# Performance work log

Measured on AMD Instinct MI355X. Metric: run time of the kernel, lower is better.

Reference implementation:

```python
import jax, jax.numpy as jnp
import numpy as np

B = 128      # puzzles per batch
CELLS = 81
N = B * CELLS
H = 96       # hidden_dim
E_SZ = 16    # embed_size
T = 16       # num_steps


def _sudoku_edges():
    r = np.arange(CELLS) // 9
    c = np.arange(CELLS) % 9
    b = (r // 3) * 3 + (c // 3)
    src, dst = [], []
    for u in range(CELLS):
        for v in range(CELLS):
            if u != v and (r[u] == r[v] or c[u] == c[v] or b[u] == b[v]):
                src.append(u)
                dst.append(v)
    return np.asarray(src, np.int32), np.asarray(dst, np.int32)


def setup_inputs() -> dict:
    key = jax.random.key(0)
    ks = jax.random.split(key, 24)
    s, d = _sudoku_edges()
    off = (np.arange(B, dtype=np.int32) * CELLS)[:, None]
    src = jnp.asarray((s[None, :] + off).reshape(-1))
    dst = jnp.asarray((d[None, :] + off).reshape(-1))
    row = jnp.asarray(np.tile(np.arange(CELLS, dtype=np.int32) // 9, B))
    col = jnp.asarray(np.tile(np.arange(CELLS, dtype=np.int32) % 9, B))
    q = jax.random.randint(ks[0], (N,), 0, 10, dtype=jnp.int32)
    labels = jax.random.randint(ks[1], (N,), 1, 10, dtype=jnp.int32)

    def lin(k, o, i):
        return (jax.random.normal(k, (o, i), jnp.float32) / np.sqrt(i)).astype(jnp.float32)

    d_emb = jax.random.normal(ks[2], (10, E_SZ), jnp.float32)
    r_emb = jax.random.normal(ks[3], (9, E_SZ), jnp.float32)
    c_emb = jax.random.normal(ks[4], (9, E_SZ), jnp.float32)
    in_W0 = lin(ks[5], H, 3 * E_SZ)
    in_W = jnp.stack([lin(ks[6 + i], H, H) for i in range(3)])   # [3,H,H]
    in_b = jnp.zeros((4, H), jnp.float32)
    msg_W0 = lin(ks[9], H, 2 * H)
    msg_W = jnp.stack([lin(ks[10 + i], H, H) for i in range(3)])
    msg_b = jnp.zeros((4, H), jnp.float32)
    # LSTMCell (no bias): input = cat(x, m) of size 2H, hidden H; gate order i,f,g,o
    W_ih = lin(ks[13], 4 * H, 2 * H)
    W_hh = lin(ks[14], 4 * H, H)
    out_W = lin(ks[15], 10, H)
    out_b = jnp.zeros((10,), jnp.float32)
    return dict(q=q, row=row, col=col, labels=labels, src=src, dst=dst,
                d_emb=d_emb, r_emb=r_emb, c_emb=c_emb,
                in_W0=in_W0, in_W=in_W, in_b=in_b,
                msg_W0=msg_W0, msg_W=msg_W, msg_b=msg_b,
                W_ih=W_ih, W_hh=W_hh, out_W=out_W, out_b=out_b)


def _mlp4(x, W0, W, b):
    # Linear,ReLU,Linear,ReLU,Linear,ReLU,Linear
    x = jax.nn.relu(x @ W0.T + b[0])
    x = jax.nn.relu(x @ W[0].T + b[1])
    x = jax.nn.relu(x @ W[1].T + b[2])
    return x @ W[2].T + b[3]


def reference(q, row, col, labels, src, dst, d_emb, r_emb, c_emb,
              in_W0, in_W, in_b, msg_W0, msg_W, msg_b,
              W_ih, W_hh, out_W, out_b):
    x = _mlp4(jnp.concatenate([d_emb[q], r_emb[row], c_emb[col]], -1),
              in_W0, in_W, in_b)                       # [N,H]
    h0 = x
    rh0 = jnp.zeros_like(x)
    rc0 = jnp.zeros_like(x)

    def step(carry, _):
        h, rh, rc = carry
        # per-edge message: MLP(cat(h_src, h_dst)), sum-aggregated into dst
        me = _mlp4(jnp.concatenate([h[src], h[dst]], -1), msg_W0, msg_W, msg_b)
        m = jax.ops.segment_sum(me, dst, num_segments=N)  # [N,H]
        gates = jnp.concatenate([x, m], -1) @ W_ih.T + rh @ W_hh.T
        i, f, g, o = jnp.split(gates, 4, axis=-1)
        nc = jax.nn.sigmoid(f) * rc + jax.nn.sigmoid(i) * jnp.tanh(g)
        nh = jax.nn.sigmoid(o) * jnp.tanh(nc)
        return (nh, nh, nc), nh

    _, hs = jax.lax.scan(step, (h0, rh0, rc0), None, length=T)  # [T,N,H]
    logits = hs @ out_W.T + out_b                               # [T,N,10]
    preds = jnp.argmax(logits, -1)                              # [T,N]
    lf = logits.reshape(-1, 10)
    lab = jnp.tile(labels, T)
    logp = jax.nn.log_softmax(lf, -1)
    loss = -jnp.mean(jnp.take_along_axis(logp, lab[:, None].astype(jnp.int32), 1))
    return preds, loss, lf
```

## Files before the change

kernel.cpp:

```cpp
#include <hip/hip_runtime.h>

#define NN 10368
#define EE 207360
#define TT 16

#define O_W0AT    0
#define O_W0BT    9216
#define O_WHHT    18432
#define O_WIHXT   55296
#define O_WCOMBT  92160
#define O_GB      129024
#define O_LOSS    129408
#define O_WIN0T   129424
#define O_WINT    134032
#define O_H       161680
#define O_C       (O_H  + NN*96)
#define O_A       (O_C  + NN*96)
#define O_BV      (O_A  + NN*96)
#define O_S2      (O_BV + NN*96)
#define O_X       (O_S2 + NN*96)
#define O_WFRAG   (O_X  + NN*96)
#define O_GX      (O_WFRAG + 27648)
#define O_WL2     O_X
#define O_WAB2    (O_X + 110592)

using bf16x8 = __attribute__((ext_vector_type(8))) short;
using f32x4  = __attribute__((ext_vector_type(4))) float;

__device__ __forceinline__ float sigm(float x){ return 1.f/(1.f + expf(-x)); }

__device__ __forceinline__ unsigned rne_bf16(float f){
  unsigned u = __float_as_uint(f);
  u += 0x7fffu + ((u >> 16) & 1u);
  return u >> 16;
}
__device__ __forceinline__ void split3(float x, short& h, short& m, short& l){
  unsigned uh = rne_bf16(x); h = (short)uh;
  float fh = __uint_as_float(uh << 16);
  float r1 = x - fh;
  unsigned um = rne_bf16(r1); m = (short)um;
  float fm = __uint_as_float(um << 16);
  float r2 = r1 - fm;
  l = (short)rne_bf16(r2);
}

__device__ __forceinline__ f32x4 mfma6(bf16x8 aH, bf16x8 aM, bf16x8 aL,
                                       bf16x8 WH, bf16x8 WM, bf16x8 WL, f32x4 acc){
  acc = __builtin_amdgcn_mfma_f32_16x16x32_bf16(aH, WH, acc, 0,0,0);
  acc = __builtin_amdgcn_mfma_f32_16x16x32_bf16(aH, WM, acc, 0,0,0);
  acc = __builtin_amdgcn_mfma_f32_16x16x32_bf16(aM, WH, acc, 0,0,0);
  acc = __builtin_amdgcn_mfma_f32_16x16x32_bf16(aH, WL, acc, 0,0,0);
  acc = __builtin_amdgcn_mfma_f32_16x16x32_bf16(aL, WH, acc, 0,0,0);
  acc = __builtin_amdgcn_mfma_f32_16x16x32_bf16(aM, WM, acc, 0,0,0);
  return acc;
}

__global__ void k_convert(float* ws, const float* msgW0, const float* Whh, const float* Wih,
                          const float* inW0, const float* inW)
{
  int i = blockIdx.x*256 + threadIdx.x;
  if (i < 9216){ int k=i/96, j=i%96; ws[O_W0AT+i] = msgW0[j*192+k];    return; } i -= 9216;
  if (i < 9216){ int k=i/96, j=i%96; ws[O_W0BT+i] = msgW0[j*192+96+k]; return; } i -= 9216;
  if (i < 36864){ int k=i/384, j=i%384; ws[O_WHHT+i]  = Whh[j*96+k];   return; } i -= 36864;
  if (i < 36864){ int k=i/384, j=i%384; ws[O_WIHXT+i] = Wih[j*192+k];  return; } i -= 36864;
  if (i < 4608){ int k=i/96, j=i%96; ws[O_WIN0T+i] = inW0[j*48+k];     return; } i -= 4608;
  if (i < 27648){ int l=i/9216, r=i%9216; int k=r/96, j=r%96;
                  ws[O_WINT+i] = inW[l*9216 + j*96 + k];               return; } i -= 27648;
  if (i == 0){ ws[O_LOSS] = 0.f; }
}

__global__ void k_wfrag(float* ws, const float* msgW)
{
  int idx = blockIdx.x*256 + threadIdx.x;
  if (idx >= 2*3*18*64) return;
  int lane = idx & 63;
  int tile = (idx >> 6) % 18;
  int lev  = (idx >> 6) / 18 % 3;
  int layer= (idx >> 6) / 54;
  int nt = tile/3, kt = tile%3;
  int nout = (lane & 15) + 16*nt;
  int q = lane >> 4;
  unsigned short* wf = (unsigned short*)(ws + O_WFRAG);
  unsigned short* dstp = wf + (size_t)(((layer*3+lev)*18 + tile)*64 + lane)*8;
  const float* W = msgW + layer*9216;
  for (int j=0;j<8;j++){
    float wv = W[nout*96 + 32*kt + 8*q + j];
    short h,m,l; split3(wv, h, m, l);
    dstp[j] = (unsigned short)(lev==0 ? h : (lev==1 ? m : l));
  }
}

__global__ void k_wcomb(float* ws, const float* Wih, const float* msgW, const float* msgb)
{
  int t = blockIdx.x*256 + threadIdx.x;
  if (t >= 36864) return;
  int j = t % 384, qq = t / 384;
  float a0=0.f,a1=0.f,a2=0.f,a3=0.f;
  for (int r=0;r<96;r+=4){
    a0 = fmaf(Wih[j*192+96+r  ], msgW[2*9216+(r  )*96+qq], a0);
    a1 = fmaf(Wih[j*192+96+r+1], msgW[2*9216+(r+1)*96+qq], a1);
    a2 = fmaf(Wih[j*192+96+r+2], msgW[2*9216+(r+2)*96+qq], a2);
    a3 = fmaf(Wih[j*192+96+r+3], msgW[2*9216+(r+3)*96+qq], a3);
  }
  ws[O_WCOMBT + qq*384 + j] = (a0+a1)+(a2+a3);
  if (qq == 0){
    float g=0.f;
    for (int r=0;r<96;r++) g = fmaf(Wih[j*192+96+r], msgb[288+r], g);
    ws[O_GB + j] = 20.f * g;
  }
}

__global__ void k_wl(float* ws)
{
  int idx = blockIdx.x*256 + threadIdx.x;
  if (idx >= 24*6*64) return;
  int L  = idx & 63;
  int ks = (idx >> 6) % 6;
  int nt = (idx >> 6) / 6;
  int col = (L & 15) + 16*nt;
  int q = L >> 4;
  unsigned short* wf = (unsigned short*)(ws + O_WL2);
  for (int j=0;j<8;j++){
    int k = 32*(ks%3) + 8*q + j;
    float wv = (ks < 3) ? ws[O_WCOMBT + k*384 + col] : ws[O_WHHT + k*384 + col];
    short h,m,l; split3(wv, h, m, l);
    wf[(size_t)(((0*24+nt)*6 + ks)*64 + L)*8 + j] = (unsigned short)h;
    wf[(size_t)(((1*24+nt)*6 + ks)*64 + L)*8 + j] = (unsigned short)m;
    wf[(size_t)(((2*24+nt)*6 + ks)*64 + L)*8 + j] = (unsigned short)l;
  }
}

__global__ void k_wab(float* ws)
{
  int idx = blockIdx.x*256 + threadIdx.x;
  if (idx >= 12*3*64) return;
  int L  = idx & 63;
  int ks = (idx >> 6) % 3;
  int nt = (idx >> 6) / 3;
  int col = (L & 15) + 16*nt;
  int q = L >> 4;
  unsigned short* wf = (unsigned short*)(ws + O_WAB2);
  for (int j=0;j<8;j++){
    int k = 32*ks + 8*q + j;
    float wv = (col < 96) ? ws[O_W0AT + k*96 + col] : ws[O_W0BT + k*96 + (col-96)];
    short h,m,l; split3(wv, h, m, l);
    wf[(size_t)(((0*12+nt)*3 + ks)*64 + L)*8 + j] = (unsigned short)h;
    wf[(size_t)(((1*12+nt)*3 + ks)*64 + L)*8 + j] = (unsigned short)m;
    wf[(size_t)(((2*12+nt)*3 + ks)*64 + L)*8 + j] = (unsigned short)l;
  }
}

__global__ __launch_bounds__(192) void k_input(float* ws,
    const int* q, const int* row, const int* col,
    const float* demb, const float* remb, const float* cemb,
    const float* inb, const float* msgb)
{
  __shared__ float ein[2][8*49];
  __shared__ float hb[2][8*97];
  int tid = threadIdx.x; int g = tid/96, j = tid%96;
  int nq = blockIdx.x*2 + g; int n0 = nq*8;

  for (int idx=j; idx<384; idx+=96){
    int i = idx/48, f = idx%48; int n = n0+i;
    float v;
    if (f < 16)      v = demb[q[n]*16 + f];
    else if (f < 32) v = remb[row[n]*16 + (f-16)];
    else             v = cemb[col[n]*16 + (f-32)];
    ein[g][i*49+f] = v;
  }
  __syncthreads();

  float acc[8];
  {
    const float* W0T = ws + O_WIN0T;
    float b0 = inb[j];
    #pragma unroll
    for (int i=0;i<8;i++) acc[i]=b0;
    #pragma unroll 2
    for (int k=0;k<48;k++){
      float w = W0T[k*96+j];
      #pragma unroll
      for (int i=0;i<8;i++) acc[i] = fmaf(w, ein[g][i*49+k], acc[i]);
    }
    #pragma unroll
    for (int i=0;i<8;i++) hb[g][i*97+j] = fmaxf(acc[i], 0.f);
  }
  __syncthreads();

  for (int l=0;l<3;l++){
    const float* WT = ws + O_WINT + l*9216;
    float bl = inb[(l+1)*96 + j];
    #pragma unroll
    for (int i=0;i<8;i++) acc[i]=bl;
    #pragma unroll 2
    for (int k=0;k<96;k++){
      float w = WT[k*96+j];
      #pragma unroll
      for (int i=0;i<8;i++) acc[i] = fmaf(w, hb[g][i*97+k], acc[i]);
    }
    __syncthreads();
    if (l < 2){
      #pragma unroll
      for (int i=0;i<8;i++) hb[g][i*97+j] = fmaxf(acc[i], 0.f);
    } else {
      #pragma unroll
      for (int i=0;i<8;i++) hb[g][i*97+j] = acc[i];
    }
    __syncthreads();
  }

  float* h = ws + O_H; float* c = ws + O_C; float* x = ws + O_X;
  #pragma unroll
  for (int i=0;i<8;i++){
    int n = n0+i;
    float vv = hb[g][i*97+j];
    h[n*96+j]=vv; x[n*96+j]=vv; c[n*96+j]=0.f;
  }
  const float* WA = ws + O_W0AT; const float* WB = ws + O_W0BT;
  float aa[8], ab[8];
  #pragma unroll
  for (int i=0;i<8;i++){ aa[i]=0.f; ab[i]=0.f; }
  #pragma unroll 2
  for (int k=0;k<96;k++){
    float wa=WA[k*96+j], wb=WB[k*96+j];
    #pragma unroll
    for (int i=0;i<8;i++){
      float hv = hb[g][i*97+k];
      aa[i]=fmaf(wa,hv,aa[i]); ab[i]=fmaf(wb,hv,ab[i]);
    }
  }
  float* A=ws+O_A; float* Bv=ws+O_BV;
  float b0v = msgb[j];
  #pragma unroll
  for (int i=0;i<8;i++){ int n=n0+i; A[n*96+j]=aa[i]; Bv[n*96+j]=ab[i]+b0v; }
}

__global__ __launch_bounds__(384) void k_gx(float* ws)
{
  __shared__ float sx[768];
  int tid = threadIdx.x;
  int nb = blockIdx.x*8;
  for (int idx = tid; idx < 768; idx += 384)
    sx[idx] = ws[O_X + (size_t)nb*96 + idx];
  float gb = ws[O_GB + tid];
  __syncthreads();
  const float* WX = ws + O_WIHXT;
  float acc[8];
  #pragma unroll
  for (int i=0;i<8;i++) acc[i] = gb;
  #pragma unroll 2
  for (int k0=0;k0<96;k0+=4){
    float4 xv[8];
    #pragma unroll
    for (int i=0;i<8;i++) xv[i] = *(const float4*)&sx[i*96+k0];
    #pragma unroll
    for (int kk=0;kk<4;kk++){
      float w = WX[(k0+kk)*384 + tid];
      #pragma unroll
      for (int i=0;i<8;i++){
        float xe = (kk==0)?xv[i].x:(kk==1)?xv[i].y:(kk==2)?xv[i].z:xv[i].w;
        acc[i] = fmaf(w, xe, acc[i]);
      }
    }
  }
  #pragma unroll
  for (int i=0;i<8;i++)
    ws[O_GX + (size_t)(nb+i)*384 + tid] = acc[i];
}

__global__ __launch_bounds__(384) void k_edge(float* ws, const int* dst, const float* msgb)
{
  __shared__ bf16x8 aF[45][64];
  int tid = threadIdx.x;
  int w = tid >> 6, L = tid & 63;
  int q = L >> 4, m = L & 15;
  int n0 = blockIdx.x*4;
  int e0 = blockIdx.x*80;
  const unsigned short* wf = (const unsigned short*)(ws + O_WFRAG);
  const float* Aact = ws + O_A;
  const float* Bact = ws + O_BV;

  for (int idx = tid; idx < 960; idx += 384){
    int mt = idx / 192;
    int kt = (idx % 192) / 64;
    int Ls = idx & 63;
    int el = mt*16 + (Ls & 15);
    int v  = dst[e0 + el];
    int n  = n0 + el/20;
    int k0 = 32*kt + 8*(Ls >> 4);
    float4 a0 = *(const float4*)(Aact + (size_t)v*96 + k0);
    float4 a1 = *(const float4*)(Aact + (size_t)v*96 + k0 + 4);
    float4 b0 = *(const float4*)(Bact + (size_t)n*96 + k0);
    float4 b1 = *(const float4*)(Bact + (size_t)n*96 + k0 + 4);
    float r[8];
    r[0]=fmaxf(a0.x+b0.x,0.f); r[1]=fmaxf(a0.y+b0.y,0.f);
    r[2]=fmaxf(a0.z+b0.z,0.f); r[3]=fmaxf(a0.w+b0.w,0.f);
    r[4]=fmaxf(a1.x+b1.x,0.f); r[5]=fmaxf(a1.y+b1.y,0.f);
    r[6]=fmaxf(a1.z+b1.z,0.f); r[7]=fmaxf(a1.w+b1.w,0.f);
    bf16x8 vh, vm, vl;
    #pragma unroll
    for (int j=0;j<8;j++){
      short hh,mm,ll; split3(r[j], hh, mm, ll);
      vh[j]=hh; vm[j]=mm; vl[j]=ll;
    }
    aF[0*15 + mt*3 + kt][Ls] = vh;
    aF[1*15 + mt*3 + kt][Ls] = vm;
    aF[2*15 + mt*3 + kt][Ls] = vl;
  }
  __syncthreads();

  f32x4 rD[5];
  {
    bf16x8 W1[3][3];
    #pragma unroll
    for (int lev=0; lev<3; lev++)
      #pragma unroll
      for (int kt=0; kt<3; kt++)
        W1[lev][kt] = ((const bf16x8*)wf)[(size_t)((0*3+lev)*18 + w*3+kt)*64 + L];
    float bb = msgb[96 + 16*w + m];
    #pragma unroll
    for (int mt=0; mt<5; mt++){
      f32x4 acc = {0.f,0.f,0.f,0.f};
      #pragma unroll
      for (int kt=0; kt<3; kt++){
        bf16x8 aH = aF[0*15+mt*3+kt][L];
        bf16x8 aM = aF[1*15+mt*3+kt][L];
        bf16x8 aL = aF[2*15+mt*3+kt][L];
        acc = mfma6(aH, aM, aL, W1[0][kt], W1[1][kt], W1[2][kt], acc);
      }
      #pragma unroll
      for (int r=0;r<4;r++) rD[mt][r] = fmaxf(acc[r] + bb, 0.f);
    }
  }
  __syncthreads();

  {
    int col = 16*w + m;
    int kt = col >> 5;
    int qp = (col & 31) >> 3;
    int j  = col & 7;
    unsigned short* af16 = (unsigned short*)&aF[0][0];
    #pragma unroll
    for (int mt=0; mt<5; mt++){
      #pragma unroll
      for (int r=0; r<4; r++){
        short hh,mm,ll; split3(rD[mt][r], hh, mm, ll);
        int Lp = 4*q + r + 16*qp;
        af16[(size_t)((0*15+mt*3+kt)*64 + Lp)*8 + j] = (unsigned short)hh;
        af16[(size_t)((1*15+mt*3+kt)*64 + Lp)*8 + j] = (unsigned short)mm;
        af16[(size_t)((2*15+mt*3+kt)*64 + Lp)*8 + j] = (unsigned short)ll;
      }
    }
  }
  __syncthreads();

  {
    bf16x8 W2[3][3];
    #pragma unroll
    for (int lev=0; lev<3; lev++)
      #pragma unroll
      for (int kt=0; kt<3; kt++)
        W2[lev][kt] = ((const bf16x8*)wf)[(size_t)((1*3+lev)*18 + w*3+kt)*64 + L];
    float bb = msgb[192 + 16*w + m];
    float sn[4] = {0.f,0.f,0.f,0.f};
    #pragma unroll
    for (int mt=0; mt<5; mt++){
      f32x4 acc = {0.f,0.f,0.f,0.f};
      #pragma unroll
      for (int kt=0; kt<3; kt++){
        bf16x8 aH = aF[0*15+mt*3+kt][L];
        bf16x8 aM = aF[1*15+mt*3+kt][L];
        bf16x8 aL = aF[2*15+mt*3+kt][L];
        acc = mfma6(aH, aM, aL, W2[0][kt], W2[1][kt], W2[2][kt], acc);
      }
      #pragma unroll
      for (int r=0;r<4;r++){
        int el = mt*16 + 4*q + r;
        float o = fmaxf(acc[r] + bb, 0.f);
        sn[el/20] += o;
      }
    }
    #pragma unroll
    for (int nd=0; nd<4; nd++){
      sn[nd] += __shfl_xor(sn[nd], 16);
      sn[nd] += __shfl_xor(sn[nd], 32);
    }
    if (L < 16){
      float* s2 = ws + O_S2;
      #pragma unroll
      for (int nd=0; nd<4; nd++)
        s2[(size_t)(n0+nd)*96 + 16*w + m] = sn[nd];
    }
  }
}

__global__ __launch_bounds__(384) void k_lstm_mf(float* ws, const int* labels,
                                                 const float* msgb,
                                                 const float* outW, const float* outb,
                                                 float* out, int t)
{
  __shared__ bf16x8 aF[3][384];
  __shared__ bf16x8 hF[3][192];
  __shared__ float sh2[16*100];
  __shared__ float lgt[160];
  int tid = threadIdx.x;
  int w = tid >> 6, L = tid & 63;
  int m = L & 15, q = L >> 4;
  int nb = blockIdx.x*16;
  const float hscale = (t == 0) ? 0.f : 1.f;

  {
    int ks = tid/64; int Ls = tid%64;
    int node = nb + (Ls & 15); int qs = Ls >> 4;
    const float* src = (ks < 3) ? (ws + O_S2 + (size_t)node*96 + 32*ks + 8*qs)
                                : (ws + O_H  + (size_t)node*96 + 32*(ks-3) + 8*qs);
    float sc = (ks < 3) ? 1.f : hscale;
    float4 v0 = *(const float4*)src;
    float4 v1 = *(const float4*)(src + 4);
    float r[8] = {v0.x,v0.y,v0.z,v0.w,v1.x,v1.y,v1.z,v1.w};
    bf16x8 vh, vm, vl;
    #pragma unroll
    for (int j=0;j<8;j++){
      short hh,mm,ll; split3(r[j]*sc, hh, mm, ll);
      vh[j]=hh; vm[j]=mm; vl[j]=ll;
    }
    aF[0][tid]=vh; aF[1][tid]=vm; aF[2][tid]=vl;
  }

  f32x4 acc[4];
  #pragma unroll
  for (int g=0; g<4; g++){
    #pragma unroll
    for (int r=0; r<4; r++)
      acc[g][r] = ws[O_GX + (size_t)(nb + q*4 + r)*384 + m + 16*(w + 6*g)];
  }
  __syncthreads();

  const bf16x8* wl = (const bf16x8*)(ws + O_WL2);
  #pragma unroll 2
  for (int ks=0; ks<6; ks++){
    bf16x8 aH = aF[0][ks*64+L], aM = aF[1][ks*64+L], aLw = aF[2][ks*64+L];
    #pragma unroll
    for (int g=0; g<4; g++){
      int nt = w + 6*g;
      bf16x8 WH = wl[(size_t)(((0*24+nt)*6 + ks)*64) + L];
      bf16x8 WM = wl[(size_t)(((1*24+nt)*6 + ks)*64) + L];
      bf16x8 WL = wl[(size_t)(((2*24+nt)*6 + ks)*64) + L];
      acc[g] = mfma6(aH, aM, aLw, WH, WM, WL, acc[g]);
    }
  }

  {
    int jj = m + 16*w;
    #pragma unroll
    for (int r=0; r<4; r++){
      int n = nb + q*4 + r;
      float ig = sigm(acc[0][r]);
      float fg = sigm(acc[1][r]);
      float gg = tanhf(acc[2][r]);
      float og = sigm(acc[3][r]);
      float cv = ws[O_C + (size_t)n*96 + jj];
      float nc = fg*cv + ig*gg;
      float nv = og*tanhf(nc);
      ws[O_C + (size_t)n*96 + jj] = nc;
      ws[O_H + (size_t)n*96 + jj] = nv;
      sh2[(q*4 + r)*100 + jj] = nv;
    }
  }
  __syncthreads();

  if (tid < 192){
    int ks = tid/64; int Ls = tid%64; int qs = Ls >> 4;
    const float* src = &sh2[(Ls & 15)*100 + 32*ks + 8*qs];
    float4 v0 = *(const float4*)src;
    float4 v1 = *(const float4*)(src + 4);
    float r[8] = {v0.x,v0.y,v0.z,v0.w,v1.x,v1.y,v1.z,v1.w};
    bf16x8 vh, vm, vl;
    #pragma unroll
    for (int j=0;j<8;j++){
      short hh,mm,ll; split3(r[j], hh, mm, ll);
      vh[j]=hh; vm[j]=mm; vl[j]=ll;
    }
    hF[0][tid]=vh; hF[1][tid]=vm; hF[2][tid]=vl;
  }
  __syncthreads();

  {
    const bf16x8* wab = (const bf16x8*)(ws + O_WAB2);
    f32x4 accA = {0.f,0.f,0.f,0.f};
    f32x4 accB = {0.f,0.f,0.f,0.f};
    #pragma unroll
    for (int ks=0; ks<3; ks++){
      bf16x8 hH = hF[0][ks*64+L], hM = hF[1][ks*64+L], hLw = hF[2][ks*64+L];
      {
        int nt = w;
        bf16x8 WH = wab[(size_t)(((0*12+nt)*3 + ks)*64) + L];
        bf16x8 WM = wab[(size_t)(((1*12+nt)*3 + ks)*64) + L];
        bf16x8 WL = wab[(size_t)(((2*12+nt)*3 + ks)*64) + L];
        accA = mfma6(hH, hM, hLw, WH, WM, WL, accA);
      }
      {
        int nt = w + 6;
        bf16x8 WH = wab[(size_t)(((0*12+nt)*3 + ks)*64) + L];
        bf16x8 WM = wab[(size_t)(((1*12+nt)*3 + ks)*64) + L];
        bf16x8 WL = wab[(size_t)(((2*12+nt)*3 + ks)*64) + L];
        accB = mfma6(hH, hM, hLw, WH, WM, WL, accB);
      }
    }
    int jj = m + 16*w;
    float b0v = msgb[jj];
    #pragma unroll
    for (int r=0; r<4; r++){
      int n = nb + q*4 + r;
      ws[O_A  + (size_t)n*96 + jj] = accA[r];
      ws[O_BV + (size_t)n*96 + jj] = accB[r] + b0v;
    }
  }

  if (tid < 160){
    int ln = tid/10, cls = tid%10;
    int n = nb + ln;
    float q0=outb[cls], q1=0.f, q2=0.f, q3v=0.f;
    const float* hr = &sh2[ln*100];
    #pragma unroll
    for (int k=0;k<96;k+=4){
      q0=fmaf(outW[cls*96+k  ],hr[k  ],q0);  q1=fmaf(outW[cls*96+k+1],hr[k+1],q1);
      q2=fmaf(outW[cls*96+k+2],hr[k+2],q2);  q3v=fmaf(outW[cls*96+k+3],hr[k+3],q3v);
    }
    float lgv = (q0+q1)+(q2+q3v);
    lgt[ln*10 + cls] = lgv;
    out[165889 + ((size_t)t*NN + n)*10 + cls] = lgv;
  }
  __syncthreads();
  if (tid < 16){
    int n = nb + tid;
    const float* Lg = &lgt[tid*10];
    float mx = Lg[0]; int bi = 0;
    #pragma unroll
    for (int cc=1;cc<10;cc++){ if (Lg[cc] > mx){ mx=Lg[cc]; bi=cc; } }
    float se = 0.f;
    #pragma unroll
    for (int cc=0;cc<10;cc++) se += expf(Lg[cc]-mx);
    int lab = labels[n];
    float lp = Lg[lab] - mx - logf(se);
    atomicAdd(ws + O_LOSS, -lp);
    out[t*NN + n] = (float)bi;
  }
}

__global__ __launch_bounds__(384) void k_lstm_valu(float* ws, const int* labels,
                                                   const float* msgb,
                                                   const float* outW, const float* outb,
                                                   float* out, int t)
{
  __shared__ float ss[768], sh[768], sx[768];
  __shared__ float lg[8*384];
  __shared__ float lh[8*97];
  __shared__ float lgt[80];
  int tid = threadIdx.x;
  int nb = blockIdx.x*8;
  const float* WC = ws + O_WCOMBT;
  const float* WH = ws + O_WHHT;
  float* h = ws + O_H; float* c = ws + O_C;
  const float hscale = (t == 0) ? 0.f : 1.f;

  for (int idx = tid; idx < 768; idx += 384){
    ss[idx] = ws[O_S2 + (size_t)nb*96 + idx];
    sh[idx] = ws[O_H  + (size_t)nb*96 + idx] * hscale;
    sx[idx] = ws[O_X + (size_t)nb*96 + idx];
  }
  float acc[8];
  float gb = ws[O_GB + tid];
  #pragma unroll
  for (int i=0;i<8;i++) acc[i] = gb;
  __syncthreads();

  {
    const float* WX = ws + O_WIHXT;
    #pragma unroll 2
    for (int k0=0;k0<96;k0+=4){
      float4 xv[8];
      #pragma unroll
      for (int i=0;i<8;i++) xv[i] = *(const float4*)&sx[i*96+k0];
      #pragma unroll
      for (int kk=0;kk<4;kk++){
        float w = WX[(k0+kk)*384 + tid];
        #pragma unroll
        for (int i=0;i<8;i++){
          float xe = (kk==0)?xv[i].x:(kk==1)?xv[i].y:(kk==2)?xv[i].z:xv[i].w;
          acc[i] = fmaf(w, xe, acc[i]);
        }
      }
    }
  }

  #pragma unroll 2
  for (int k0=0;k0<96;k0+=4){
    float4 sv[8], rv[8];
    #pragma unroll
    for (int i=0;i<8;i++){
      sv[i] = *(const float4*)&ss[i*96+k0];
      rv[i] = *(const float4*)&sh[i*96+k0];
    }
    #pragma unroll
    for (int kk=0;kk<4;kk++){
      float cw = WC[(k0+kk)*384 + tid];
      float hw = WH[(k0+kk)*384 + tid];
      #pragma unroll
      for (int i=0;i<8;i++){
        float se = (kk==0)?sv[i].x:(kk==1)?sv[i].y:(kk==2)?sv[i].z:sv[i].w;
        float re = (kk==0)?rv[i].x:(kk==1)?rv[i].y:(kk==2)?rv[i].z:rv[i].w;
        acc[i] = fmaf(cw, se, fmaf(hw, re, acc[i]));
      }
    }
  }
  #pragma unroll
  for (int i=0;i<8;i++) lg[i*384 + tid] = acc[i];
  __syncthreads();

  #pragma unroll
  for (int half=0; half<2; half++){
    int p = tid + half*384;
    int i = p/96, jj = p%96;
    int n = nb + i;
    float ig = sigm(lg[i*384 + jj]);
    float fg = sigm(lg[i*384 + 96 + jj]);
    float gg = tanhf(lg[i*384 + 192 + jj]);
    float og = sigm(lg[i*384 + 288 + jj]);
    float cv = c[(size_t)n*96 + jj];
    float nc = fg*cv + ig*gg;
    float nv = og*tanhf(nc);
    c[(size_t)n*96 + jj] = nc;
    h[(size_t)n*96 + jj] = nv;
    lh[i*97 + jj] = nv;
  }
  __syncthreads();

  {
    const float* WA = ws + O_W0AT; const float* WB = ws + O_W0BT;
    int q3 = tid/96, jj = tid%96;
    int i0 = q3*2;
    float aa0=0.f, aa1=0.f, ab0=0.f, ab1=0.f;
    #pragma unroll 2
    for (int k=0;k<96;k++){
      float wa = WA[k*96+jj], wb = WB[k*96+jj];
      float h0v = lh[i0*97 + k], h1v = lh[(i0+1)*97 + k];
      aa0 = fmaf(wa, h0v, aa0); ab0 = fmaf(wb, h0v, ab0);
      aa1 = fmaf(wa, h1v, aa1); ab1 = fmaf(wb, h1v, ab1);
    }
    float b0v = msgb[jj];
    float* Aa = ws + O_A; float* Bb = ws + O_BV;
    Aa[(size_t)(nb+i0)*96 + jj]   = aa0; Bb[(size_t)(nb+i0)*96 + jj]   = ab0 + b0v;
    Aa[(size_t)(nb+i0+1)*96 + jj] = aa1; Bb[(size_t)(nb+i0+1)*96 + jj] = ab1 + b0v;
  }

  if (tid < 80){
    int ln = tid/10, cls = tid%10;
    int n = nb + ln;
    float q0=outb[cls], q1=0.f, q2=0.f, q3v=0.f;
    const float* hr = &lh[ln*97];
    #pragma unroll
    for (int k=0;k<96;k+=4){
      q0=fmaf(outW[cls*96+k  ],hr[k  ],q0);  q1=fmaf(outW[cls*96+k+1],hr[k+1],q1);
      q2=fmaf(outW[cls*96+k+2],hr[k+2],q2);  q3v=fmaf(outW[cls*96+k+3],hr[k+3],q3v);
    }
    float lgv = (q0+q1)+(q2+q3v);
    lgt[ln*10 + cls] = lgv;
    out[165889 + ((size_t)t*NN + n)*10 + cls] = lgv;
  }
  __syncthreads();
  if (tid < 8){
    int n = nb + tid;
    const float* Lg = &lgt[tid*10];
    float mx = Lg[0]; int bi = 0;
    #pragma unroll
    for (int cc=1;cc<10;cc++){ if (Lg[cc] > mx){ mx=Lg[cc]; bi=cc; } }
    float se = 0.f;
    #pragma unroll
    for (int cc=0;cc<10;cc++) se += expf(Lg[cc]-mx);
    int lab = labels[n];
    float lp = Lg[lab] - mx - logf(se);
    atomicAdd(ws + O_LOSS, -lp);
    out[t*NN + n] = (float)bi;
  }
}

__global__ void k_final(float* ws, float* out){
  if (threadIdx.x == 0 && blockIdx.x == 0)
    out[165888] = ws[O_LOSS] / (float)(TT*NN);
}

extern "C" void kernel_launch(void* const* d_in, const int* in_sizes, int n_in,
                              void* d_out, int out_size, void* d_ws, size_t ws_size,
                              hipStream_t stream)
{
  (void)in_sizes; (void)n_in; (void)out_size;
  const int* q      = (const int*)d_in[0];
  const int* row    = (const int*)d_in[1];
  const int* col    = (const int*)d_in[2];
  const int* labels = (const int*)d_in[3];
  const int* dst    = (const int*)d_in[5];
  const float* demb  = (const float*)d_in[6];
  const float* remb  = (const float*)d_in[7];
  const float* cemb  = (const float*)d_in[8];
  const float* inW0  = (const float*)d_in[9];
  const float* inW   = (const float*)d_in[10];
  const float* inb   = (const float*)d_in[11];
  const float* msgW0 = (const float*)d_in[12];
  const float* msgW  = (const float*)d_in[13];
  const float* msgb  = (const float*)d_in[14];
  const float* Wih   = (const float*)d_in[15];
  const float* Whh   = (const float*)d_in[16];
  const float* outW  = (const float*)d_in[17];
  const float* outb  = (const float*)d_in[18];

  float* ws  = (float*)d_ws;
  float* out = (float*)d_out;

  const size_t need_gx = ((size_t)O_GX + (size_t)NN*384) * sizeof(float);
  const int use_mf = (ws_size >= need_gx) ? 1 : 0;

  hipLaunchKernelGGL(k_convert, dim3(487), dim3(256), 0, stream,
                     ws, msgW0, Whh, Wih, inW0, inW);
  hipLaunchKernelGGL(k_wfrag, dim3(27), dim3(256), 0, stream, ws, msgW);
  hipLaunchKernelGGL(k_wcomb, dim3(144), dim3(256), 0, stream, ws, Wih, msgW, msgb);
  hipLaunchKernelGGL(k_input, dim3(648), dim3(192), 0, stream,
                     ws, q, row, col, demb, remb, cemb, inb, msgb);
  if (use_mf){
    hipLaunchKernelGGL(k_gx, dim3(1296), dim3(384), 0, stream, ws);
    hipLaunchKernelGGL(k_wl,  dim3(36), dim3(256), 0, stream, ws);
    hipLaunchKernelGGL(k_wab, dim3(9),  dim3(256), 0, stream, ws);
  }
  for (int t=0; t<TT; ++t){
    hipLaunchKernelGGL(k_edge, dim3(EE/80), dim3(384), 0, stream, ws, dst, msgb);
    if (use_mf)
      hipLaunchKernelGGL(k_lstm_mf, dim3(NN/16), dim3(384), 0, stream,
                         ws, labels, msgb, outW, outb, out, t);
    else
      hipLaunchKernelGGL(k_lstm_valu, dim3(1296), dim3(384), 0, stream,
                         ws, labels, msgb, outW, outb, out, t);
  }
  hipLaunchKernelGGL(k_final, dim3(1), dim3(64), 0, stream, ws, out);
}
```

Before: 1.628 ms.

## Move input MLP and input-gate projection onto split-bf16 MFMA in one kernel

```diff
diff --git a/kernel.cpp b/kernel.cpp
--- a/kernel.cpp
+++ b/kernel.cpp
@@ -23,6 +23,9 @@
 #define O_GX      (O_WFRAG + 27648)
 #define O_WL2     O_X
 #define O_WAB2    (O_X + 110592)
+#define SF_WIN0   O_S2
+#define SF_WIN    (O_S2 + 9216)
+#define SF_WX     (O_S2 + 50688)
 
 using bf16x8 = __attribute__((ext_vector_type(8))) short;
 using f32x4  = __attribute__((ext_vector_type(4))) float;
@@ -150,6 +153,215 @@
   }
 }
 
+__global__ void k_wfin(float* ws)
+{
+  int idx = blockIdx.x*256 + threadIdx.x;
+  if (idx >= 138*64) return;
+  int L = idx & 63;
+  int f = idx >> 6;
+  int q = L >> 4, mcol = L & 15;
+  if (f < 12){
+    int nt = f >> 1, ks = f & 1;
+    int col = mcol + 16*nt;
+    unsigned short* wp = (unsigned short*)(ws + SF_WIN0);
+    for (int j=0;j<8;j++){
+      int k = 32*ks + 8*q + j;
+      float v = (k < 48) ? ws[O_WIN0T + k*96 + col] : 0.f;
+      short h,m,l; split3(v,h,m,l);
+      wp[(size_t)((0*12 + f)*64 + L)*8 + j] = (unsigned short)h;
+      wp[(size_t)((1*12 + f)*64 + L)*8 + j] = (unsigned short)m;
+      wp[(size_t)((2*12 + f)*64 + L)*8 + j] = (unsigned short)l;
+    }
+  } else if (f < 66){
+    int f2 = f - 12;
+    int l = f2/18, r2 = f2%18;
+    int nt = r2/3, ks = r2%3;
+    int col = mcol + 16*nt;
+    unsigned short* wp = (unsigned short*)(ws + SF_WIN);
+    for (int j=0;j<8;j++){
+      int k = 32*ks + 8*q + j;
+      float v = ws[O_WINT + l*9216 + k*96 + col];
+      short h,m,l2; split3(v,h,m,l2);
+      wp[(size_t)((0*54 + f2)*64 + L)*8 + j] = (unsigned short)h;
+      wp[(size_t)((1*54 + f2)*64 + L)*8 + j] = (unsigned short)m;
+      wp[(size_t)((2*54 + f2)*64 + L)*8 + j] = (unsigned short)l2;
+    }
+  } else {
+    int f3 = f - 66;
+    int nt = f3/3, ks = f3%3;
+    int col = mcol + 16*nt;
+    unsigned short* wp = (unsigned short*)(ws + SF_WX);
+    for (int j=0;j<8;j++){
+      int k = 32*ks + 8*q + j;
+      float v = ws[O_WIHXT + k*384 + col];
+      short h,m,l2; split3(v,h,m,l2);
+      wp[(size_t)((0*72 + f3)*64 + L)*8 + j] = (unsigned short)h;
+      wp[(size_t)((1*72 + f3)*64 + L)*8 + j] = (unsigned short)m;
+      wp[(size_t)((2*72 + f3)*64 + L)*8 + j] = (unsigned short)l2;
+    }
+  }
+}
+
+__global__ __launch_bounds__(384) void k_input_mf(float* ws,
+    const int* q, const int* row, const int* col,
+    const float* demb, const float* remb, const float* cemb,
+    const float* inb, const float* msgb)
+{
+  __shared__ float eintile[16*49];
+  __shared__ bf16x8 fA[3][3][64];
+  __shared__ bf16x8 fB[3][3][64];
+  int tid = threadIdx.x;
+  int w = tid >> 6, L = tid & 63;
+  int m = L & 15, qd = L >> 4;
+  int nb = blockIdx.x*16;
+  int colw = 16*w + m;
+
+  for (int idx = tid; idx < 768; idx += 384){
+    int ni = idx/48, f = idx%48;
+    int n = nb + ni;
+    float v;
+    if (f < 16)      v = demb[q[n]*16 + f];
+    else if (f < 32) v = remb[row[n]*16 + (f-16)];
+    else             v = cemb[col[n]*16 + (f-32)];
+    eintile[ni*49 + f] = v;
+  }
+  __syncthreads();
+
+  if (tid < 128){
+    int ks = tid >> 6, Ls = tid & 63;
+    int node = Ls & 15, qs = Ls >> 4;
+    bf16x8 vh, vm, vl;
+    #pragma unroll
+    for (int j=0;j<8;j++){
+      int k = 32*ks + 8*qs + j;
+      float v = (k < 48) ? eintile[node*49 + k] : 0.f;
+      short hh,mm,ll; split3(v, hh, mm, ll);
+      vh[j]=hh; vm[j]=mm; vl[j]=ll;
+    }
+    fA[0][ks][Ls]=vh; fA[1][ks][Ls]=vm; fA[2][ks][Ls]=vl;
+  }
+  __syncthreads();
+
+  int kt = colw >> 5, qp = (colw & 31) >> 3, jc = colw & 7;
+
+  f32x4 acc;
+  {
+    float b0 = inb[colw];
+    acc[0]=b0; acc[1]=b0; acc[2]=b0; acc[3]=b0;
+    const bf16x8* W = (const bf16x8*)(ws + SF_WIN0);
+    #pragma unroll
+    for (int ks=0; ks<2; ks++){
+      acc = mfma6(fA[0][ks][L], fA[1][ks][L], fA[2][ks][L],
+                  W[(size_t)((0*12 + w*2+ks)*64) + L],
+                  W[(size_t)((1*12 + w*2+ks)*64) + L],
+                  W[(size_t)((2*12 + w*2+ks)*64) + L], acc);
+    }
+  }
+  {
+    unsigned short* bp = (unsigned short*)&fB[0][0][0];
+    #pragma unroll
+    for (int r=0;r<4;r++){
+      float v = fmaxf(acc[r], 0.f);
+      short hh,mm,ll; split3(v, hh, mm, ll);
+      int Lp = 4*qd + r + 16*qp;
+      bp[(size_t)((0*3+kt)*64 + Lp)*8 + jc] = (unsigned short)hh;
+      bp[(size_t)((1*3+kt)*64 + Lp)*8 + jc] = (unsigned short)mm;
+      bp[(size_t)((2*3+kt)*64 + Lp)*8 + jc] = (unsigned short)ll;
+    }
+  }
+  __syncthreads();
+
+  #pragma unroll
+  for (int l=0; l<3; l++){
+    bf16x8 (*src)[3][64] = (l & 1) ? fA : fB;
+    bf16x8 (*dstb)[3][64] = (l & 1) ? fB : fA;
+    float bl = inb[(l+1)*96 + colw];
+    acc[0]=bl; acc[1]=bl; acc[2]=bl; acc[3]=bl;
+    const bf16x8* W = (const bf16x8*)(ws + SF_WIN);
+    #pragma unroll
+    for (int ks=0; ks<3; ks++){
+      acc = mfma6(src[0][ks][L], src[1][ks][L], src[2][ks][L],
+                  W[(size_t)((0*54 + l*18 + w*3+ks)*64) + L],
+                  W[(size_t)((1*54 + l*18 + w*3+ks)*64) + L],
+                  W[(size_t)((2*54 + l*18 + w*3+ks)*64) + L], acc);
+    }
+    if (l < 2){
+      unsigned short* bp = (unsigned short*)&dstb[0][0][0];
+      #pragma unroll
+      for (int r=0;r<4;r++){
+        float v = fmaxf(acc[r], 0.f);
+        short hh,mm,ll; split3(v, hh, mm, ll);
+        int Lp = 4*qd + r + 16*qp;
+        bp[(size_t)((0*3+kt)*64 + Lp)*8 + jc] = (unsigned short)hh;
+        bp[(size_t)((1*3+kt)*64 + Lp)*8 + jc] = (unsigned short)mm;
+        bp[(size_t)((2*3+kt)*64 + Lp)*8 + jc] = (unsigned short)ll;
+      }
+      __syncthreads();
+    }
+  }
+  {
+    unsigned short* bp = (unsigned short*)&fA[0][0][0];
+    #pragma unroll
+    for (int r=0;r<4;r++){
+      int n = nb + 4*qd + r;
+      ws[O_H + (size_t)n*96 + colw] = acc[r];
+      ws[O_C + (size_t)n*96 + colw] = 0.f;
+      short hh,mm,ll; split3(acc[r], hh, mm, ll);
+      int Lp = 4*qd + r + 16*qp;
+      bp[(size_t)((0*3+kt)*64 + Lp)*8 + jc] = (unsigned short)hh;
+      bp[(size_t)((1*3+kt)*64 + Lp)*8 + jc] = (unsigned short)mm;
+      bp[(size_t)((2*3+kt)*64 + Lp)*8 + jc] = (unsigned short)ll;
+    }
+  }
+  __syncthreads();
+
+  {
+    const bf16x8* wab = (const bf16x8*)(ws + O_WAB2);
+    f32x4 accA = {0.f,0.f,0.f,0.f};
+    f32x4 accB = {0.f,0.f,0.f,0.f};
+    #pragma unroll
+    for (int ks=0; ks<3; ks++){
+      bf16x8 hH = fA[0][ks][L], hM = fA[1][ks][L], hL = fA[2][ks][L];
+      accA = mfma6(hH, hM, hL,
+                   wab[(size_t)(((0*12+w)*3 + ks)*64) + L],
+                   wab[(size_t)(((1*12+w)*3 + ks)*64) + L],
+                   wab[(size_t)(((2*12+w)*3 + ks)*64) + L], accA);
+      accB = mfma6(hH, hM, hL,
+                   wab[(size_t)(((0*12+w+6)*3 + ks)*64) + L],
+                   wab[(size_t)(((1*12+w+6)*3 + ks)*64) + L],
+                   wab[(size_t)(((2*12+w+6)*3 + ks)*64) + L], accB);
+    }
+    float b0v = msgb[colw];
+    #pragma unroll
+    for (int r=0; r<4; r++){
+      int n = nb + 4*qd + r;
+      ws[O_A  + (size_t)n*96 + colw] = accA[r];
+      ws[O_BV + (size_t)n*96 + colw] = accB[r] + b0v;
+    }
+  }
+
+  {
+    const bf16x8* wx = (const bf16x8*)(ws + SF_WX);
+    #pragma unroll
+    for (int g=0; g<4; g++){
+      int nt = w + 6*g;
+      int c384 = m + 16*nt;
+      float gbv = ws[O_GB + c384];
+      f32x4 ag; ag[0]=gbv; ag[1]=gbv; ag[2]=gbv; ag[3]=gbv;
+      #pragma unroll
+      for (int ks=0; ks<3; ks++){
+        ag = mfma6(fA[0][ks][L], fA[1][ks][L], fA[2][ks][L],
+                   wx[(size_t)((0*72 + nt*3+ks)*64) + L],
+                   wx[(size_t)((1*72 + nt*3+ks)*64) + L],
+                   wx[(size_t)((2*72 + nt*3+ks)*64) + L], ag);
+      }
+      #pragma unroll
+      for (int r=0; r<4; r++)
+        ws[O_GX + (size_t)(nb + 4*qd + r)*384 + c384] = ag[r];
+    }
+  }
+}
+
 __global__ __launch_bounds__(192) void k_input(float* ws,
     const int* q, const int* row, const int* col,
     const float* demb, const float* remb, const float* cemb,
@@ -233,39 +445,6 @@
   float b0v = msgb[j];
   #pragma unroll
   for (int i=0;i<8;i++){ int n=n0+i; A[n*96+j]=aa[i]; Bv[n*96+j]=ab[i]+b0v; }
-}
-
-__global__ __launch_bounds__(384) void k_gx(float* ws)
-{
-  __shared__ float sx[768];
-  int tid = threadIdx.x;
-  int nb = blockIdx.x*8;
-  for (int idx = tid; idx < 768; idx += 384)
-    sx[idx] = ws[O_X + (size_t)nb*96 + idx];
-  float gb = ws[O_GB + tid];
-  __syncthreads();
-  const float* WX = ws + O_WIHXT;
-  float acc[8];
-  #pragma unroll
-  for (int i=0;i<8;i++) acc[i] = gb;
-  #pragma unroll 2
-  for (int k0=0;k0<96;k0+=4){
-    float4 xv[8];
-    #pragma unroll
-    for (int i=0;i<8;i++) xv[i] = *(const float4*)&sx[i*96+k0];
-    #pragma unroll
-    for (int kk=0;kk<4;kk++){
-      float w = WX[(k0+kk)*384 + tid];
-      #pragma unroll
-      for (int i=0;i<8;i++){
-        float xe = (kk==0)?xv[i].x:(kk==1)?xv[i].y:(kk==2)?xv[i].z:xv[i].w;
-        acc[i] = fmaf(w, xe, acc[i]);
-      }
-    }
-  }
-  #pragma unroll
-  for (int i=0;i<8;i++)
-    ws[O_GX + (size_t)(nb+i)*384 + tid] = acc[i];
 }
 
 __global__ __launch_bounds__(384) void k_edge(float* ws, const int* dst, const float* msgb)
@@ -315,18 +494,16 @@
     #pragma unroll
     for (int lev=0; lev<3; lev++)
       #pragma unroll
-      for (int kt=0; kt<3; kt++)
-        W1[lev][kt] = ((const bf16x8*)wf)[(size_t)((0*3+lev)*18 + w*3+kt)*64 + L];
+      for (int kt2=0; kt2<3; kt2++)
+        W1[lev][kt2] = ((const bf16x8*)wf)[(size_t)((0*3+lev)*18 + w*3+kt2)*64 + L];
     float bb = msgb[96 + 16*w + m];
     #pragma unroll
     for (int mt=0; mt<5; mt++){
       f32x4 acc = {0.f,0.f,0.f,0.f};
       #pragma unroll
-      for (int kt=0; kt<3; kt++){
-        bf16x8 aH = aF[0*15+mt*3+kt][L];
-        bf16x8 aM = aF[1*15+mt*3+kt][L];
-        bf16x8 aL = aF[2*15+mt*3+kt][L];
-        acc = mfma6(aH, aM, aL, W1[0][kt], W1[1][kt], W1[2][kt], acc);
+      for (int kt2=0; kt2<3; kt2++){
+        acc = mfma6(aF[0*15+mt*3+kt2][L], aF[1*15+mt*3+kt2][L], aF[2*15+mt*3+kt2][L],
+                    W1[0][kt2], W1[1][kt2], W1[2][kt2], acc);
       }
       #pragma unroll
       for (int r=0;r<4;r++) rD[mt][r] = fmaxf(acc[r] + bb, 0.f);
@@ -335,10 +512,10 @@
   __syncthreads();
 
   {
-    int col = 16*w + m;
-    int kt = col >> 5;
-    int qp = (col & 31) >> 3;
-    int j  = col & 7;
+    int colc = 16*w + m;
+    int kt2 = colc >> 5;
+    int qp = (colc & 31) >> 3;
+    int j  = colc & 7;
     unsigned short* af16 = (unsigned short*)&aF[0][0];
     #pragma unroll
     for (int mt=0; mt<5; mt++){
@@ -346,9 +523,9 @@
       for (int r=0; r<4; r++){
         short hh,mm,ll; split3(rD[mt][r], hh, mm, ll);
         int Lp = 4*q + r + 16*qp;
-        af16[(size_t)((0*15+mt*3+kt)*64 + Lp)*8 + j] = (unsigned short)hh;
-        af16[(size_t)((1*15+mt*3+kt)*64 + Lp)*8 + j] = (unsigned short)mm;
-        af16[(size_t)((2*15+mt*3+kt)*64 + Lp)*8 + j] = (unsigned short)ll;
+        af16[(size_t)((0*15+mt*3+kt2)*64 + Lp)*8 + j] = (unsigned short)hh;
+        af16[(size_t)((1*15+mt*3+kt2)*64 + Lp)*8 + j] = (unsigned short)mm;
+        af16[(size_t)((2*15+mt*3+kt2)*64 + Lp)*8 + j] = (unsigned short)ll;
       }
     }
   }
@@ -359,19 +536,17 @@
     #pragma unroll
     for (int lev=0; lev<3; lev++)
       #pragma unroll
-      for (int kt=0; kt<3; kt++)
-        W2[lev][kt] = ((const bf16x8*)wf)[(size_t)((1*3+lev)*18 + w*3+kt)*64 + L];
+      for (int kt2=0; kt2<3; kt2++)
+        W2[lev][kt2] = ((const bf16x8*)wf)[(size_t)((1*3+lev)*18 + w*3+kt2)*64 + L];
     float bb = msgb[192 + 16*w + m];
     float sn[4] = {0.f,0.f,0.f,0.f};
     #pragma unroll
     for (int mt=0; mt<5; mt++){
       f32x4 acc = {0.f,0.f,0.f,0.f};
       #pragma unroll
-      for (int kt=0; kt<3; kt++){
-        bf16x8 aH = aF[0*15+mt*3+kt][L];
-        bf16x8 aM = aF[1*15+mt*3+kt][L];
-        bf16x8 aL = aF[2*15+mt*3+kt][L];
-        acc = mfma6(aH, aM, aL, W2[0][kt], W2[1][kt], W2[2][kt], acc);
+      for (int kt2=0; kt2<3; kt2++){
+        acc = mfma6(aF[0*15+mt*3+kt2][L], aF[1*15+mt*3+kt2][L], aF[2*15+mt*3+kt2][L],
+                    W2[0][kt2], W2[1][kt2], W2[2][kt2], acc);
       }
       #pragma unroll
       for (int r=0;r<4;r++){
@@ -492,20 +667,14 @@
     #pragma unroll
     for (int ks=0; ks<3; ks++){
       bf16x8 hH = hF[0][ks*64+L], hM = hF[1][ks*64+L], hLw = hF[2][ks*64+L];
-      {
-        int nt = w;
-        bf16x8 WH = wab[(size_t)(((0*12+nt)*3 + ks)*64) + L];
-        bf16x8 WM = wab[(size_t)(((1*12+nt)*3 + ks)*64) + L];
-        bf16x8 WL = wab[(size_t)(((2*12+nt)*3 + ks)*64) + L];
-        accA = mfma6(hH, hM, hLw, WH, WM, WL, accA);
-      }
-      {
-        int nt = w + 6;
-        bf16x8 WH = wab[(size_t)(((0*12+nt)*3 + ks)*64) + L];
-        bf16x8 WM = wab[(size_t)(((1*12+nt)*3 + ks)*64) + L];
-        bf16x8 WL = wab[(size_t)(((2*12+nt)*3 + ks)*64) + L];
-        accB = mfma6(hH, hM, hLw, WH, WM, WL, accB);
-      }
+      accA = mfma6(hH, hM, hLw,
+                   wab[(size_t)(((0*12+w)*3 + ks)*64) + L],
+                   wab[(size_t)(((1*12+w)*3 + ks)*64) + L],
+                   wab[(size_t)(((2*12+w)*3 + ks)*64) + L], accA);
+      accB = mfma6(hH, hM, hLw,
+                   wab[(size_t)(((0*12+w+6)*3 + ks)*64) + L],
+                   wab[(size_t)(((1*12+w+6)*3 + ks)*64) + L],
+                   wab[(size_t)(((2*12+w+6)*3 + ks)*64) + L], accB);
     }
     int jj = m + 16*w;
     float b0v = msgb[jj];
@@ -724,12 +893,15 @@
                      ws, msgW0, Whh, Wih, inW0, inW);
   hipLaunchKernelGGL(k_wfrag, dim3(27), dim3(256), 0, stream, ws, msgW);
   hipLaunchKernelGGL(k_wcomb, dim3(144), dim3(256), 0, stream, ws, Wih, msgW, msgb);
-  hipLaunchKernelGGL(k_input, dim3(648), dim3(192), 0, stream,
-                     ws, q, row, col, demb, remb, cemb, inb, msgb);
   if (use_mf){
-    hipLaunchKernelGGL(k_gx, dim3(1296), dim3(384), 0, stream, ws);
+    hipLaunchKernelGGL(k_wfin, dim3(35), dim3(256), 0, stream, ws);
     hipLaunchKernelGGL(k_wl,  dim3(36), dim3(256), 0, stream, ws);
     hipLaunchKernelGGL(k_wab, dim3(9),  dim3(256), 0, stream, ws);
+    hipLaunchKernelGGL(k_input_mf, dim3(648), dim3(384), 0, stream,
+                       ws, q, row, col, demb, remb, cemb, inb, msgb);
+  } else {
+    hipLaunchKernelGGL(k_input, dim3(648), dim3(192), 0, stream,
+                       ws, q, row, col, demb, remb, cemb, inb, msgb);
   }
   for (int t=0; t<TT; ++t){
     hipLaunchKernelGGL(k_edge, dim3(EE/80), dim3(384), 0, stream, ws, dst, msgb);
```

New measurement: 1.578 ms. -3.1%, faster.
